# Optimization experiments

Hardware: AMD Instinct MI355X
Metric: run time of the kernel (lower is better)

Reference implementation:

```python
import jax, jax.numpy as jnp
import numpy as np

B, FQ, CH0, N = 128, 318, 109, 1024
M = N + 1  # node slots incl. zero 'null child' slot at index 0


def setup_inputs() -> dict:
    key = jax.random.key(0)
    ks = jax.random.split(key, 18)
    def rn(k, shape, scale=0.05):
        return jax.random.normal(k, shape, dtype=jnp.float32) * scale
    return {
        "x": rn(ks[0], (B, FQ, M), 1.0),                       # raw node features
        "idx": jax.random.randint(ks[1], (B, 3 * N), 0, M),    # (node,left,right) triples, 0 = null
        "W_enc": rn(ks[2], (CH0, FQ)), "b_enc": rn(ks[3], (CH0,)),
        "W1": rn(ks[4], (512, CH0, 3)), "b1": rn(ks[5], (512,)),
        "W2": rn(ks[6], (256, 512, 3)), "b2": rn(ks[7], (256,)),
        "W3": rn(ks[8], (128, 256, 3)), "b3": rn(ks[9], (128,)),
        "Wh1": rn(ks[10], (128, 128)), "bh1": rn(ks[11], (128,)),
        "Wh2": rn(ks[12], (64, 128)), "bh2": rn(ks[13], (64,)),
        "Wh3": rn(ks[14], (32, 64)), "bh3": rn(ks[15], (32,)),
        "Wh4": rn(ks[16], (1, 32)), "bh4": rn(ks[17], (1,)),
    }


def _btc(trees, idx, W, b):
    # trees: (B, C, M); idx: (B, 3N). Gather triples then k=3 stride=3 conv.
    g = jax.vmap(lambda t, i: t[:, i])(trees, idx)           # (B, C, 3N)
    g = g.reshape(g.shape[0], g.shape[1], -1, 3)             # (B, C, N, 3)
    out = jnp.einsum('bcnk,ock->bon', g, W) + b[None, :, None]
    zero = jnp.zeros((out.shape[0], out.shape[1], 1), out.dtype)
    return jnp.concatenate([zero, out], axis=2)              # (B, O, N+1)


def _tree_norm_act(t):
    # TreeLayerNorm: normalize per tree over (channels, nodes); torch.std is unbiased
    mean = jnp.mean(t, axis=(1, 2), keepdims=True)
    std = jnp.std(t, axis=(1, 2), ddof=1, keepdims=True)
    return jax.nn.relu((t - mean) / (std + 1e-5))


def reference(x, idx, W_enc, b_enc, W1, b1, W2, b2, W3, b3,
              Wh1, bh1, Wh2, bh2, Wh3, bh3, Wh4, bh4):
    # QueryEncoder: per-node linear 318 -> 109, keep null slot zero
    t = jnp.einsum('bfm,cf->bcm', x, W_enc) + b_enc[None, :, None]
    t = t.at[:, :, 0].set(0.0)
    t = _tree_norm_act(_btc(t, idx, W1, b1))
    t = _tree_norm_act(_btc(t, idx, W2, b2))
    t = _tree_norm_act(_btc(t, idx, W3, b3))
    h = jnp.max(t, axis=2)                                   # DynamicPooling: (B, 128)
    h = jax.nn.relu(h @ Wh1.T + bh1)
    h = jax.nn.relu(h @ Wh2.T + bh2)
    h = jax.nn.relu(h @ Wh3.T + bh3)
    return h @ Wh4.T + bh4                                   # (B, 1)
```

## Files before the change

### kernel.cpp

```cpp
#include <hip/hip_runtime.h>
#include <hip/hip_bf16.h>
#include <math.h>

#define B_   128
#define FQ_  318
#define CH0_ 109
#define NN_  1024
#define MM_  1025
#define C1_  512
#define C2_  256
#define C3_  128
#define C0P_ 128

typedef _Float16 f16x8 __attribute__((ext_vector_type(8)));
typedef float    f32x4 __attribute__((ext_vector_type(4)));

#define GLOAD_LDS16(g, l) __builtin_amdgcn_global_load_lds( \
    (const __attribute__((address_space(1))) void*)(g),     \
    (__attribute__((address_space(3))) void*)(l), 16, 0, 0)
#define GLOAD_LDS4(g, l) __builtin_amdgcn_global_load_lds(  \
    (const __attribute__((address_space(1))) void*)(g),     \
    (__attribute__((address_space(3))) void*)(l), 4, 0, 0)

__device__ __forceinline__ int lds_qoff(int row, int q) {
    return row * 32 + (((q ^ ((row >> 1) & 3)) & 3) << 3);
}

template <int C_IN, int C_IN_PAD, int C_OUT>
__global__ __launch_bounds__(256) void wprep_kernel(
    const float* __restrict__ W, _Float16* __restrict__ Wh, _Float16* __restrict__ Wl)
{
    constexpr int KP = 3 * C_IN_PAD;
    const int id = blockIdx.x * 256 + threadIdx.x;
    if (id >= C_OUT * KP) return;
    const int o = id / KP, k = id - o * KP;
    const int kk = k / C_IN_PAD, c = k - kk * C_IN_PAD;
    const float v = (c < C_IN) ? W[((size_t)o * C_IN + c) * 3 + kk] : 0.f;
    const _Float16 h = (_Float16)v;
    Wh[id] = h;
    Wl[id] = (_Float16)(v - (float)h);
}

__global__ __launch_bounds__(256) void wprep_enc_kernel(
    const float* __restrict__ We, _Float16* __restrict__ Wh, _Float16* __restrict__ Wl)
{
    const int id = blockIdx.x * 256 + threadIdx.x;
    if (id >= 128 * 320) return;
    const int c = id / 320, f = id - c * 320;
    const float v = (c < CH0_ && f < FQ_) ? We[(size_t)c * FQ_ + f] : 0.f;
    const _Float16 h = (_Float16)v;
    Wh[id] = h;
    Wl[id] = (_Float16)(v - (float)h);
}

__global__ __launch_bounds__(512, 2) void enc_mfma_kernel(
    const float* __restrict__ x,
    const _Float16* __restrict__ Weh, const _Float16* __restrict__ Wel,
    const float* __restrict__ benc, _Float16* __restrict__ t0)
{
    constexpr int MROW = 264;
    constexpr int NCE  = 10;
    __shared__ __align__(16) float    XS[2][32 * MROW];
    __shared__ __align__(16) _Float16 WhS[2][128 * 32];
    __shared__ __align__(16) _Float16 WlS[2][128 * 32];

    const int tid  = threadIdx.x;
    const int lane = tid & 63, wid = tid >> 6;
    const int wr = wid >> 1, wc = wid & 1;
    const int lrow = lane & 15, lkg = lane >> 4;

    const int nwg  = 4 * B_;
    const int cpx  = nwg >> 3;
    const int swz  = (blockIdx.x & 7) * cpx + (blockIdx.x >> 3);
    const int b    = swz >> 2;
    const int mt   = swz & 3;
    const int m_base = mt * 256;

    auto stageX = [&](int ch, int buf) {
        const int f0 = ch * 32;
#pragma unroll
        for (int s = 0; s < 4; ++s) {
            const int floc = wid * 4 + s;
            int f = f0 + floc;
            if (f > FQ_ - 1) f = FQ_ - 1;
            const float* src = x + ((size_t)b * FQ_ + f) * MM_ + 1 + m_base;
            float* dst = &XS[buf][floc * MROW];
#pragma unroll
            for (int u = 0; u < 4; ++u)
                GLOAD_LDS4(src + u * 64 + lane, dst + u * 64);
        }
    };

    auto stageWE = [&](int ch, int buf) {
        const int baseRow = wid * 16;
        const int row  = baseRow + (lane >> 2);
        const int qp   = lane & 3;
        const int qsrc = qp ^ ((row >> 1) & 3);
        const size_t goff = (size_t)row * 320 + ch * 32 + qsrc * 8;
        GLOAD_LDS16(Weh + goff, &WhS[buf][baseRow * 32]);
        GLOAD_LDS16(Wel + goff, &WlS[buf][baseRow * 32]);
    };

    f32x4 acc[4][4];
#pragma unroll
    for (int i = 0; i < 4; ++i)
#pragma unroll
        for (int j = 0; j < 4; ++j) acc[i][j] = (f32x4){0.f, 0.f, 0.f, 0.f};

    auto compute = [&](int buf) {
        f16x8 ah[4], al[4];
#pragma unroll
        for (int i = 0; i < 4; ++i) {
            const int mloc = wr * 64 + i * 16 + lrow;
            const float* rp = &XS[buf][(lkg * 8) * MROW + mloc];
            f16x8 vh, vl;
#pragma unroll
            for (int j = 0; j < 8; ++j) {
                const float v = rp[j * MROW];
                const _Float16 h = (_Float16)v;
                vh[j] = h;
                vl[j] = (_Float16)(v - (float)h);
            }
            ah[i] = vh;
            al[i] = vl;
        }
        __builtin_amdgcn_s_setprio(1);
#pragma unroll
        for (int j = 0; j < 4; ++j) {
            const int cr  = wc * 64 + j * 16 + lrow;
            const int off = lds_qoff(cr, lkg);
            const f16x8 bh = *reinterpret_cast<const f16x8*>(&WhS[buf][off]);
            const f16x8 bl = *reinterpret_cast<const f16x8*>(&WlS[buf][off]);
#pragma unroll
            for (int i = 0; i < 4; ++i)
                acc[i][j] = __builtin_amdgcn_mfma_f32_16x16x32_f16(ah[i], bh, acc[i][j], 0, 0, 0);
#pragma unroll
            for (int i = 0; i < 4; ++i)
                acc[i][j] = __builtin_amdgcn_mfma_f32_16x16x32_f16(al[i], bh, acc[i][j], 0, 0, 0);
#pragma unroll
            for (int i = 0; i < 4; ++i)
                acc[i][j] = __builtin_amdgcn_mfma_f32_16x16x32_f16(ah[i], bl, acc[i][j], 0, 0, 0);
        }
        __builtin_amdgcn_s_setprio(0);
    };

    stageX(0, 0);
    stageWE(0, 0);
    __syncthreads();
    for (int ch = 0; ch < NCE; ++ch) {
        const int buf = ch & 1;
        if (ch + 1 < NCE) {
            stageX(ch + 1, buf ^ 1);
            stageWE(ch + 1, buf ^ 1);
        }
        compute(buf);
        __syncthreads();
    }

    _Float16* outb = t0 + (size_t)b * MM_ * C0P_;
#pragma unroll
    for (int i = 0; i < 4; ++i) {
        const int vm = m_base + wr * 64 + i * 16 + lkg * 4;
#pragma unroll
        for (int j = 0; j < 4; ++j) {
            const int c = wc * 64 + j * 16 + lrow;
            const float bb = (c < CH0_) ? benc[c] : 0.f;
#pragma unroll
            for (int r = 0; r < 4; ++r) {
                const float v = (c < CH0_) ? (acc[i][j][r] + bb) : 0.f;
                outb[(size_t)(vm + r + 1) * C0P_ + c] = (_Float16)v;
            }
        }
    }
    if (mt == 0) {
        for (int c = tid; c < C0P_; c += 512) outb[c] = (_Float16)0.f;
    }
}

template <int C_IN_STRIDE, int C_OUT, int OTILE, bool NORM>
__global__ __launch_bounds__(1024, 4) void conv_mfma_kernel(
    const _Float16* __restrict__ tin, const int* __restrict__ idx,
    const _Float16* __restrict__ Wh,
    const float* __restrict__ bias,
    const double* __restrict__ stats_in, const int prev_count,
    double* __restrict__ stats_out, _Float16* __restrict__ tout)
{
    constexpr int KP   = 3 * C_IN_STRIDE;
    constexpr int NC   = KP / 32;
    constexpr int CPC  = C_IN_STRIDE / 32;
    constexpr int OTB  = C_OUT / OTILE;
    constexpr int OF   = OTILE / 64;
    static_assert(KP % 32 == 0 && (CPC & (CPC - 1)) == 0, "bad pad");
    static_assert(OTILE == 128 || OTILE == 256, "otile");

    __shared__ __align__(16) _Float16 GhS[2][256 * 32];
    __shared__ __align__(16) _Float16 WhS[2][OTILE * 32];
    __shared__ int idxs[768];
    __shared__ float s_norm[2];
    __shared__ double redS[16], redQ[16];

    const int tid = threadIdx.x;

    const int nwg  = 4 * OTB * B_;
    const int cpx  = nwg >> 3;
    const int orig = blockIdx.x;
    const int swz  = (orig & 7) * cpx + (orig >> 3);
    const int b    = swz / (4 * OTB);
    const int rr   = swz - b * (4 * OTB);
    const int mt   = rr / OTB;
    const int ot   = rr - mt * OTB;
    const int n_base = mt * 256;
    const int o0     = ot * OTILE;

    if (tid < 768) {
        idxs[tid] = idx[(size_t)b * (3 * NN_) + n_base * 3 + tid];
    }
    if (NORM && tid == 0) {
        const double s = stats_in[2 * b], q = stats_in[2 * b + 1];
        const double meand = s / prev_count;
        const double var   = (q - s * s / prev_count) / (prev_count - 1);
        s_norm[0] = (float)meand;
        s_norm[1] = (float)(1.0 / (sqrt(var) + 1e-5));
    }
    __syncthreads();
    const float mean = NORM ? s_norm[0] : 0.f;
    const float inv  = NORM ? s_norm[1] : 1.f;

    const _Float16* tb = tin + (size_t)b * MM_ * C_IN_STRIDE;
    const int gn = tid >> 2, gh = tid & 3;
    const int lane = tid & 63, wid = tid >> 6;
    const int wr = wid >> 2, wc = wid & 3;
    const int lrow = lane & 15, lkg = lane >> 4;

    f16x8 gv;

    auto load_chunk = [&](int ch) {
        const int kk = ch / CPC;
        const int c0 = (ch & (CPC - 1)) << 5;
        const int r  = idxs[gn * 3 + kk];
        gv = *reinterpret_cast<const f16x8*>(tb + (size_t)r * C_IN_STRIDE + c0 + gh * 8);
    };

    auto stageW = [&](int ch, int buf) {
        if constexpr (OTILE == 256) {
            const int baseRow = wid * 16;
            const int row  = baseRow + (lane >> 2);
            const int qp   = lane & 3;
            const int qsrc = qp ^ ((row >> 1) & 3);
            const size_t goff = (size_t)(o0 + row) * KP + ch * 32 + qsrc * 8;
            GLOAD_LDS16(Wh + goff, &WhS[buf][baseRow * 32]);
        } else {
            if (wid < 8) {
                const int baseRow = wid * 16;
                const int row  = baseRow + (lane >> 2);
                const int qp   = lane & 3;
                const int qsrc = qp ^ ((row >> 1) & 3);
                const size_t goff = (size_t)(o0 + row) * KP + ch * 32 + qsrc * 8;
                GLOAD_LDS16(Wh + goff, &WhS[buf][baseRow * 32]);
            }
        }
    };

    auto store_chunk = [&](int buf) {
        const int off = lds_qoff(gn, gh);
        if constexpr (!NORM) {
            *reinterpret_cast<f16x8*>(&GhS[buf][off]) = gv;
        } else {
            f16x8 vh;
#pragma unroll
            for (int e = 0; e < 8; ++e) {
                float v = (float)gv[e];
                v = fmaxf(0.f, v - mean);
                vh[e] = (_Float16)v;
            }
            *reinterpret_cast<f16x8*>(&GhS[buf][off]) = vh;
        }
    };

    f32x4 acc[4][OF];
#pragma unroll
    for (int i = 0; i < 4; ++i)
#pragma unroll
        for (int j = 0; j < OF; ++j) acc[i][j] = (f32x4){0.f, 0.f, 0.f, 0.f};

    auto compute_chunk = [&](int buf) {
        f16x8 ah[4];
#pragma unroll
        for (int f = 0; f < 4; ++f) {
            const int ar  = wr * 64 + f * 16 + lrow;
            const int off = lds_qoff(ar, lkg);
            ah[f] = *reinterpret_cast<const f16x8*>(&GhS[buf][off]);
        }
        __builtin_amdgcn_s_setprio(1);
#pragma unroll
        for (int j = 0; j < OF; ++j) {
            const int br  = wc * (OTILE / 4) + j * 16 + lrow;
            const int off = lds_qoff(br, lkg);
            const f16x8 bh = *reinterpret_cast<const f16x8*>(&WhS[buf][off]);
#pragma unroll
            for (int i = 0; i < 4; ++i)
                acc[i][j] = __builtin_amdgcn_mfma_f32_16x16x32_f16(ah[i], bh, acc[i][j], 0, 0, 0);
        }
        __builtin_amdgcn_s_setprio(0);
    };

    stageW(0, 0);
    load_chunk(0);
    store_chunk(0);
    __syncthreads();
    for (int ch = 0; ch < NC; ++ch) {
        const int buf = ch & 1;
        if (ch + 1 < NC) {
            stageW(ch + 1, buf ^ 1);
            load_chunk(ch + 1);
        }
        compute_chunk(buf);
        if (ch + 1 < NC) store_chunk(buf ^ 1);
        __syncthreads();
    }

    float bv[OF];
#pragma unroll
    for (int j = 0; j < OF; ++j) bv[j] = bias[o0 + wc * (OTILE / 4) + j * 16 + lrow];

    double s = 0.0, q = 0.0;
    _Float16* outb = tout + (size_t)b * MM_ * C_OUT;
#pragma unroll
    for (int i = 0; i < 4; ++i) {
        const int nrow = n_base + wr * 64 + i * 16 + lkg * 4;
#pragma unroll
        for (int j = 0; j < OF; ++j) {
            const int o = o0 + wc * (OTILE / 4) + j * 16 + lrow;
#pragma unroll
            for (int r = 0; r < 4; ++r) {
                const float v = fmaf(acc[i][j][r], inv, bv[j]);
                outb[(size_t)(nrow + r + 1) * C_OUT + o] = (_Float16)v;
                s += (double)v;
                q += (double)v * (double)v;
            }
        }
    }
    if (mt == 0) {
        for (int o = tid; o < OTILE; o += 1024) outb[o0 + o] = (_Float16)0.f;
    }

#pragma unroll
    for (int off = 32; off > 0; off >>= 1) {
        s += __shfl_down(s, off);
        q += __shfl_down(q, off);
    }
    if (lane == 0) { redS[wid] = s; redQ[wid] = q; }
    __syncthreads();
    if (tid == 0) {
        double ts = 0.0, tq = 0.0;
#pragma unroll
        for (int w = 0; w < 16; ++w) { ts += redS[w]; tq += redQ[w]; }
        atomicAdd(&stats_out[2 * b], ts);
        atomicAdd(&stats_out[2 * b + 1], tq);
    }
}

__global__ __launch_bounds__(1024) void pool_head_kernel(
    const _Float16* __restrict__ t3, const double* __restrict__ stats3,
    const float* __restrict__ Wh1, const float* __restrict__ bh1,
    const float* __restrict__ Wh2, const float* __restrict__ bh2,
    const float* __restrict__ Wh3, const float* __restrict__ bh3,
    const float* __restrict__ Wh4, const float* __restrict__ bh4,
    float* __restrict__ out)
{
    __shared__ float red[8][128];
    __shared__ float hs[128], h1s[128], h2s[64], h3s[32];
    const int b = blockIdx.x;
    const int o = threadIdx.x & 127, mg = threadIdx.x >> 7;

    const double ssum = stats3[2 * b], ssq = stats3[2 * b + 1];
    const double cnt  = (double)C3_ * (double)MM_;
    const double meand = ssum / cnt;
    const double var   = (ssq - ssum * ssum / cnt) / (cnt - 1.0);
    const float mean = (float)meand;
    const float inv  = (float)(1.0 / (sqrt(var) + 1e-5));

    const _Float16* tb = t3 + (size_t)b * MM_ * C3_;
    float best = 0.f;
    for (int m = mg; m < MM_; m += 8) {
        const float v = fmaxf(0.f, ((float)tb[(size_t)m * C3_ + o] - mean) * inv);
        best = fmaxf(best, v);
    }
    red[mg][o] = best;
    __syncthreads();

    const int t = threadIdx.x;
    if (t < 128) {
        float h = red[0][t];
#pragma unroll
        for (int g = 1; g < 8; ++g) h = fmaxf(h, red[g][t]);
        hs[t] = h;
    }
    __syncthreads();

    if (t < 128) {
        float a1 = bh1[t];
        for (int i = 0; i < 128; ++i) a1 = fmaf(Wh1[t * 128 + i], hs[i], a1);
        h1s[t] = fmaxf(a1, 0.f);
    }
    __syncthreads();

    if (t < 64) {
        float a2 = bh2[t];
        for (int i = 0; i < 128; ++i) a2 = fmaf(Wh2[t * 128 + i], h1s[i], a2);
        h2s[t] = fmaxf(a2, 0.f);
    }
    __syncthreads();

    if (t < 32) {
        float a3 = bh3[t];
        for (int i = 0; i < 64; ++i) a3 = fmaf(Wh3[t * 64 + i], h2s[i], a3);
        h3s[t] = fmaxf(a3, 0.f);
    }
    __syncthreads();

    if (t == 0) {
        float a4 = bh4[0];
        for (int i = 0; i < 32; ++i) a4 = fmaf(Wh4[i], h3s[i], a4);
        out[b] = a4;
    }
}

extern "C" void kernel_launch(void* const* d_in, const int* in_sizes, int n_in,
                              void* d_out, int out_size, void* d_ws, size_t ws_size,
                              hipStream_t stream)
{
    const float* x    = (const float*)d_in[0];
    const int*   idx  = (const int*)d_in[1];
    const float* Wenc = (const float*)d_in[2];
    const float* benc = (const float*)d_in[3];
    const float* W1   = (const float*)d_in[4];
    const float* b1   = (const float*)d_in[5];
    const float* W2   = (const float*)d_in[6];
    const float* b2   = (const float*)d_in[7];
    const float* W3   = (const float*)d_in[8];
    const float* b3   = (const float*)d_in[9];
    const float* Wh1  = (const float*)d_in[10];
    const float* bh1  = (const float*)d_in[11];
    const float* Wh2  = (const float*)d_in[12];
    const float* bh2  = (const float*)d_in[13];
    const float* Wh3  = (const float*)d_in[14];
    const float* bh3  = (const float*)d_in[15];
    const float* Wh4  = (const float*)d_in[16];
    const float* bh4  = (const float*)d_in[17];
    float* out = (float*)d_out;

    char* ws = (char*)d_ws;
    double* stats = (double*)ws;
    _Float16* w1h = (_Float16*)(ws + 8192);
    _Float16* w1l = (_Float16*)(ws + 401408);
    _Float16* w2h = (_Float16*)(ws + 794624);
    _Float16* w2l = (_Float16*)(ws + 1581056);
    _Float16* w3h = (_Float16*)(ws + 2367488);
    _Float16* w3l = (_Float16*)(ws + 2564096);
    _Float16* wEh = (_Float16*)(ws + 2760704);
    _Float16* wEl = (_Float16*)(ws + 2842624);
    const size_t offA = 2924544;
    const size_t offB = offA + (size_t)B_ * MM_ * C2_ * sizeof(_Float16);
    _Float16* t0 = (_Float16*)(ws + offA);
    _Float16* t1 = (_Float16*)(ws + offB);
    _Float16* t2 = (_Float16*)(ws + offA);
    _Float16* t3 = (_Float16*)(ws + offB);

    hipMemsetAsync(stats, 0, 3 * B_ * 2 * sizeof(double), stream);

    wprep_kernel<CH0_, 128, C1_><<<dim3((C1_ * 384 + 255) / 256), dim3(256), 0, stream>>>(W1, w1h, w1l);
    wprep_kernel<C1_,  C1_, C2_><<<dim3((C2_ * 1536 + 255) / 256), dim3(256), 0, stream>>>(W2, w2h, w2l);
    wprep_kernel<C2_,  C2_, C3_><<<dim3((C3_ * 768 + 255) / 256), dim3(256), 0, stream>>>(W3, w3h, w3l);
    wprep_enc_kernel<<<dim3((128 * 320 + 255) / 256), dim3(256), 0, stream>>>(Wenc, wEh, wEl);

    enc_mfma_kernel<<<dim3(4 * B_), dim3(512), 0, stream>>>(x, wEh, wEl, benc, t0);

    conv_mfma_kernel<C0P_, C1_, 256, false><<<dim3(4 * 2 * B_), dim3(1024), 0, stream>>>(
        t0, idx, w1h, b1, nullptr, 1, stats + 0, t1);

    conv_mfma_kernel<C1_, C2_, 256, true><<<dim3(4 * 1 * B_), dim3(1024), 0, stream>>>(
        t1, idx, w2h, b2, stats + 0, C1_ * MM_, stats + 2 * B_, t2);

    conv_mfma_kernel<C2_, C3_, 128, true><<<dim3(4 * 1 * B_), dim3(1024), 0, stream>>>(
        t2, idx, w3h, b3, stats + 2 * B_, C2_ * MM_, stats + 4 * B_, t3);

    pool_head_kernel<<<dim3(B_), dim3(1024), 0, stream>>>(
        t3, stats + 4 * B_, Wh1, bh1, Wh2, bh2, Wh3, bh3, Wh4, bh4, out);
}
```

Baseline: 365.1 us.

## Fuse max-pooling into last conv and drop low-half X term in encoder

```diff
diff --git a/kernel.cpp b/kernel.cpp
--- a/kernel.cpp
+++ b/kernel.cpp
@@ -108,21 +108,15 @@
         for (int j = 0; j < 4; ++j) acc[i][j] = (f32x4){0.f, 0.f, 0.f, 0.f};
 
     auto compute = [&](int buf) {
-        f16x8 ah[4], al[4];
+        f16x8 ah[4];
 #pragma unroll
         for (int i = 0; i < 4; ++i) {
             const int mloc = wr * 64 + i * 16 + lrow;
             const float* rp = &XS[buf][(lkg * 8) * MROW + mloc];
-            f16x8 vh, vl;
-#pragma unroll
-            for (int j = 0; j < 8; ++j) {
-                const float v = rp[j * MROW];
-                const _Float16 h = (_Float16)v;
-                vh[j] = h;
-                vl[j] = (_Float16)(v - (float)h);
-            }
+            f16x8 vh;
+#pragma unroll
+            for (int j = 0; j < 8; ++j) vh[j] = (_Float16)rp[j * MROW];
             ah[i] = vh;
-            al[i] = vl;
         }
         __builtin_amdgcn_s_setprio(1);
 #pragma unroll
@@ -136,9 +130,6 @@
                 acc[i][j] = __builtin_amdgcn_mfma_f32_16x16x32_f16(ah[i], bh, acc[i][j], 0, 0, 0);
 #pragma unroll
             for (int i = 0; i < 4; ++i)
-                acc[i][j] = __builtin_amdgcn_mfma_f32_16x16x32_f16(al[i], bh, acc[i][j], 0, 0, 0);
-#pragma unroll
-            for (int i = 0; i < 4; ++i)
                 acc[i][j] = __builtin_amdgcn_mfma_f32_16x16x32_f16(ah[i], bl, acc[i][j], 0, 0, 0);
         }
         __builtin_amdgcn_s_setprio(0);
@@ -177,13 +168,14 @@
     }
 }
 
-template <int C_IN_STRIDE, int C_OUT, int OTILE, bool NORM>
+template <int C_IN_STRIDE, int C_OUT, int OTILE, bool NORM, bool FUSE_MAX>
 __global__ __launch_bounds__(1024, 4) void conv_mfma_kernel(
     const _Float16* __restrict__ tin, const int* __restrict__ idx,
     const _Float16* __restrict__ Wh,
     const float* __restrict__ bias,
     const double* __restrict__ stats_in, const int prev_count,
-    double* __restrict__ stats_out, _Float16* __restrict__ tout)
+    double* __restrict__ stats_out, _Float16* __restrict__ tout,
+    float* __restrict__ pmax)
 {
     constexpr int KP   = 3 * C_IN_STRIDE;
     constexpr int NC   = KP / 32;
@@ -192,6 +184,7 @@
     constexpr int OF   = OTILE / 64;
     static_assert(KP % 32 == 0 && (CPC & (CPC - 1)) == 0, "bad pad");
     static_assert(OTILE == 128 || OTILE == 256, "otile");
+    static_assert(!FUSE_MAX || OTILE == 128, "fuse needs single o-tile");
 
     __shared__ __align__(16) _Float16 GhS[2][256 * 32];
     __shared__ __align__(16) _Float16 WhS[2][OTILE * 32];
@@ -324,6 +317,10 @@
     for (int j = 0; j < OF; ++j) bv[j] = bias[o0 + wc * (OTILE / 4) + j * 16 + lrow];
 
     double s = 0.0, q = 0.0;
+    float cm[OF];
+#pragma unroll
+    for (int j = 0; j < OF; ++j) cm[j] = -3.0e38f;
+
     _Float16* outb = tout + (size_t)b * MM_ * C_OUT;
 #pragma unroll
     for (int i = 0; i < 4; ++i) {
@@ -334,14 +331,38 @@
 #pragma unroll
             for (int r = 0; r < 4; ++r) {
                 const float v = fmaf(acc[i][j][r], inv, bv[j]);
-                outb[(size_t)(nrow + r + 1) * C_OUT + o] = (_Float16)v;
                 s += (double)v;
                 q += (double)v * (double)v;
+                if constexpr (FUSE_MAX) cm[j] = fmaxf(cm[j], v);
+                else outb[(size_t)(nrow + r + 1) * C_OUT + o] = (_Float16)v;
             }
         }
     }
-    if (mt == 0) {
-        for (int o = tid; o < OTILE; o += 1024) outb[o0 + o] = (_Float16)0.f;
+    if constexpr (!FUSE_MAX) {
+        if (mt == 0) {
+            for (int o = tid; o < OTILE; o += 1024) outb[o0 + o] = (_Float16)0.f;
+        }
+    }
+
+    if constexpr (FUSE_MAX) {
+        __shared__ float pmS[16][32];
+#pragma unroll
+        for (int j = 0; j < OF; ++j) {
+            cm[j] = fmaxf(cm[j], __shfl_xor(cm[j], 16));
+            cm[j] = fmaxf(cm[j], __shfl_xor(cm[j], 32));
+        }
+        if (lane < 16) {
+            pmS[wid][lane]      = cm[0];
+            pmS[wid][16 + lane] = cm[1];
+        }
+        __syncthreads();
+        if (tid < 128) {
+            const int o = tid, pwc = o >> 5, rem = o & 31;
+            float m = pmS[0 * 4 + pwc][rem];
+#pragma unroll
+            for (int w2 = 1; w2 < 4; ++w2) m = fmaxf(m, pmS[w2 * 4 + pwc][rem]);
+            pmax[((size_t)b * 4 + mt) * 128 + o] = m;
+        }
     }
 
 #pragma unroll
@@ -360,18 +381,16 @@
     }
 }
 
-__global__ __launch_bounds__(1024) void pool_head_kernel(
-    const _Float16* __restrict__ t3, const double* __restrict__ stats3,
+__global__ __launch_bounds__(128) void pool_head_kernel(
+    const float* __restrict__ pmax, const double* __restrict__ stats3,
     const float* __restrict__ Wh1, const float* __restrict__ bh1,
     const float* __restrict__ Wh2, const float* __restrict__ bh2,
     const float* __restrict__ Wh3, const float* __restrict__ bh3,
     const float* __restrict__ Wh4, const float* __restrict__ bh4,
     float* __restrict__ out)
 {
-    __shared__ float red[8][128];
     __shared__ float hs[128], h1s[128], h2s[64], h3s[32];
-    const int b = blockIdx.x;
-    const int o = threadIdx.x & 127, mg = threadIdx.x >> 7;
+    const int b = blockIdx.x, t = threadIdx.x;
 
     const double ssum = stats3[2 * b], ssq = stats3[2 * b + 1];
     const double cnt  = (double)C3_ * (double)MM_;
@@ -380,29 +399,16 @@
     const float mean = (float)meand;
     const float inv  = (float)(1.0 / (sqrt(var) + 1e-5));
 
-    const _Float16* tb = t3 + (size_t)b * MM_ * C3_;
-    float best = 0.f;
-    for (int m = mg; m < MM_; m += 8) {
-        const float v = fmaxf(0.f, ((float)tb[(size_t)m * C3_ + o] - mean) * inv);
-        best = fmaxf(best, v);
-    }
-    red[mg][o] = best;
-    __syncthreads();
-
-    const int t = threadIdx.x;
-    if (t < 128) {
-        float h = red[0][t];
-#pragma unroll
-        for (int g = 1; g < 8; ++g) h = fmaxf(h, red[g][t]);
-        hs[t] = h;
-    }
-    __syncthreads();
-
-    if (t < 128) {
-        float a1 = bh1[t];
-        for (int i = 0; i < 128; ++i) a1 = fmaf(Wh1[t * 128 + i], hs[i], a1);
-        h1s[t] = fmaxf(a1, 0.f);
-    }
+    float m = 0.f;
+#pragma unroll
+    for (int mt = 0; mt < 4; ++mt)
+        m = fmaxf(m, pmax[((size_t)b * 4 + mt) * 128 + t]);
+    hs[t] = fmaxf(0.f, (m - mean) * inv);
+    __syncthreads();
+
+    float a1 = bh1[t];
+    for (int i = 0; i < 128; ++i) a1 = fmaf(Wh1[t * 128 + i], hs[i], a1);
+    h1s[t] = fmaxf(a1, 0.f);
     __syncthreads();
 
     if (t < 64) {
@@ -460,12 +466,12 @@
     _Float16* w3l = (_Float16*)(ws + 2564096);
     _Float16* wEh = (_Float16*)(ws + 2760704);
     _Float16* wEl = (_Float16*)(ws + 2842624);
-    const size_t offA = 2924544;
+    float*    pmax = (float*)(ws + 2924544);
+    const size_t offA = 3186688;
     const size_t offB = offA + (size_t)B_ * MM_ * C2_ * sizeof(_Float16);
     _Float16* t0 = (_Float16*)(ws + offA);
     _Float16* t1 = (_Float16*)(ws + offB);
     _Float16* t2 = (_Float16*)(ws + offA);
-    _Float16* t3 = (_Float16*)(ws + offB);
 
     hipMemsetAsync(stats, 0, 3 * B_ * 2 * sizeof(double), stream);
 
@@ -476,15 +482,15 @@
 
     enc_mfma_kernel<<<dim3(4 * B_), dim3(512), 0, stream>>>(x, wEh, wEl, benc, t0);
 
-    conv_mfma_kernel<C0P_, C1_, 256, false><<<dim3(4 * 2 * B_), dim3(1024), 0, stream>>>(
-        t0, idx, w1h, b1, nullptr, 1, stats + 0, t1);
-
-    conv_mfma_kernel<C1_, C2_, 256, true><<<dim3(4 * 1 * B_), dim3(1024), 0, stream>>>(
-        t1, idx, w2h, b2, stats + 0, C1_ * MM_, stats + 2 * B_, t2);
-
-    conv_mfma_kernel<C2_, C3_, 128, true><<<dim3(4 * 1 * B_), dim3(1024), 0, stream>>>(
-        t2, idx, w3h, b3, stats + 2 * B_, C2_ * MM_, stats + 4 * B_, t3);
-
-    pool_head_kernel<<<dim3(B_), dim3(1024), 0, stream>>>(
-        t3, stats + 4 * B_, Wh1, bh1, Wh2, bh2, Wh3, bh3, Wh4, bh4, out);
-}
+    conv_mfma_kernel<C0P_, C1_, 256, false, false><<<dim3(4 * 2 * B_), dim3(1024), 0, stream>>>(
+        t0, idx, w1h, b1, nullptr, 1, stats + 0, t1, nullptr);
+
+    conv_mfma_kernel<C1_, C2_, 256, true, false><<<dim3(4 * 1 * B_), dim3(1024), 0, stream>>>(
+        t1, idx, w2h, b2, stats + 0, C1_ * MM_, stats + 2 * B_, t2, nullptr);
+
+    conv_mfma_kernel<C2_, C3_, 128, true, true><<<dim3(4 * 1 * B_), dim3(1024), 0, stream>>>(
+        t2, idx, w3h, b3, stats + 2 * B_, C2_ * MM_, stats + 4 * B_, nullptr, pmax);
+
+    pool_head_kernel<<<dim3(B_), dim3(128), 0, stream>>>(
+        pmax, stats + 4 * B_, Wh1, bh1, Wh2, bh2, Wh3, bh3, Wh4, bh4, out);
+}
```

Result: faster. 335.6 us (-8.1%).
